# Kernel optimization log

Measured on AMD Instinct MI355X. Metric: run time of the kernel, lower is better.

Reference implementation:

```python
import jax, jax.numpy as jnp
import numpy as np

WS = 8  # window size
NH = 8  # num heads
LN_EPS = 1e-5


def _rel_pos_index(ws):
    coords = np.stack(np.meshgrid(np.arange(ws), np.arange(ws), indexing='ij'))  # [2,ws,ws]
    cf = coords.reshape(2, -1)                      # [2, ws*ws]
    rc = (cf[:, :, None] - cf[:, None, :]).transpose(1, 2, 0).astype(np.int64)  # [N,N,2]
    rc[..., 0] += ws - 1
    rc[..., 1] += ws - 1
    rc[..., 0] *= 2 * ws - 1
    return jnp.asarray(rc.sum(-1), dtype=jnp.int32)  # [N,N]


def setup_inputs() -> dict:
    key = jax.random.key(0)
    B, C, H, W = 8, 256, 128, 128
    hid = 4 * C
    ks = jax.random.split(key, 16)
    rn = lambda k, shape, s=0.02: (jax.random.normal(k, shape, jnp.float32) * s)
    return {
        'x': jax.random.normal(ks[0], (B, H * W, C), jnp.float32),
        'feature': jax.random.normal(ks[1], (B, C, H, W), jnp.float32),
        'Wq': rn(ks[2], (C, C)), 'bq': jnp.zeros((C,), jnp.float32),
        'Wk': rn(ks[3], (C, C)), 'bk': jnp.zeros((C,), jnp.float32),
        'Wv': rn(ks[4], (C, C)), 'bv': jnp.zeros((C,), jnp.float32),
        'Wo': rn(ks[5], (C, C)), 'bo': jnp.zeros((C,), jnp.float32),
        'rpb_table': rn(ks[6], ((2 * WS - 1) ** 2, NH)),
        'g1': jnp.ones((C,), jnp.float32), 'beta1': jnp.zeros((C,), jnp.float32),
        'g2': jnp.ones((C,), jnp.float32), 'beta2': jnp.zeros((C,), jnp.float32),
        'Wm1': rn(ks[7], (C, hid)), 'bm1': jnp.zeros((hid,), jnp.float32),
        'Wm2': rn(ks[8], (hid, C)), 'bm2': jnp.zeros((C,), jnp.float32),
        'Wu1': rn(ks[9], (C, C)), 'bu1': jnp.zeros((C,), jnp.float32),
        'Wu2': rn(ks[10], (C, C)), 'bu2': jnp.zeros((C,), jnp.float32),
        'rel_idx': _rel_pos_index(WS),
    }


def _gelu(t):
    return jax.nn.gelu(t, approximate=False)  # torch nn.GELU default (erf)


def _ln(t, g, b):
    mu = jnp.mean(t, axis=-1, keepdims=True)
    var = jnp.var(t, axis=-1, keepdims=True)
    return (t - mu) * jax.lax.rsqrt(var + LN_EPS) * g + b


def reference(x, feature, Wq, bq, Wk, bk, Wv, bv, Wo, bo, rpb_table,
              g1, beta1, g2, beta2, Wm1, bm1, Wm2, bm2, Wu1, bu1, Wu2, bu2,
              rel_idx):
    B, C, H, W = feature.shape
    ws, nh = WS, NH
    hd = C // nh
    scale = hd ** -0.5

    # unary potential: Linear -> GELU -> Linear on x [B, HW, C]
    unary = _gelu(x @ Wu1 + bu1) @ Wu2 + bu2

    # window partition of feature
    f = feature.reshape(B, C, H * W).transpose(0, 2, 1)  # [B, HW, C]
    pad_h = (-H) % ws
    pad_w = (-W) % ws
    fimg = f.reshape(B, H, W, C)
    if pad_h or pad_w:
        fimg = jnp.pad(fimg, ((0, 0), (0, pad_h), (0, pad_w), (0, 0)))
    Hp, Wp_ = H + pad_h, W + pad_w
    win = fimg.reshape(B, Hp // ws, ws, Wp_ // ws, ws, C)
    win = win.transpose(0, 1, 3, 2, 4, 5).reshape(-1, ws * ws, C)  # [nW, N, C]

    xn = _ln(win, g1, beta1)
    N = ws * ws
    q = (xn @ Wq + bq).reshape(-1, N, nh, hd).transpose(0, 2, 1, 3)  # [nW, h, N, d]
    k = (xn @ Wk + bk).reshape(-1, N, nh, hd).transpose(0, 2, 1, 3)
    v = (xn @ Wv + bv).reshape(-1, N, nh, hd).transpose(0, 2, 1, 3)

    attn = jnp.einsum('whnd,whmd->whnm', q, k) * scale
    bias = rpb_table[rel_idx.reshape(-1)].reshape(N, N, nh).transpose(2, 0, 1)  # [h,N,N]
    attn = jax.nn.softmax(attn + bias[None], axis=-1)
    o = jnp.einsum('whnm,whmd->whnd', attn, v)
    o = o.transpose(0, 2, 1, 3).reshape(-1, N, C) @ Wo + bo  # [nW, N, C]

    # window reverse
    rev = o.reshape(B, Hp // ws, Wp_ // ws, ws, ws, C)
    rev = rev.transpose(0, 1, 3, 2, 4, 5).reshape(B, Hp, Wp_, C)
    if pad_h or pad_w:
        rev = rev[:, :H, :W, :]
    rev = rev.reshape(B, H * W, C)

    x2 = unary + rev
    out = x2 + (_gelu(_ln(x2, g2, beta2) @ Wm1 + bm1) @ Wm2 + bm2)
    return out
```

## Files before the change

kernel.cpp:

```cpp
#include <hip/hip_runtime.h>
#include <cmath>


typedef unsigned short u16;
typedef unsigned int u32;
typedef __bf16 bf16x8 __attribute__((ext_vector_type(8)));
typedef float f32x4 __attribute__((ext_vector_type(4)));

#define EPI_NONE 0
#define EPI_GELU 1
#define EPI_WINREV 2
#define EPI_ADD 3

#define MTOK 131072
#define CC 256
#define HWC 16384

__device__ __forceinline__ float b2f(u16 u) {
    union { u32 i; float f; } x; x.i = ((u32)u) << 16; return x.f;
}
__device__ __forceinline__ u16 f2b(float f) {
    union { float f; u32 i; } x; x.f = f;
    u32 r = x.i + 0x7fffu + ((x.i >> 16) & 1u);
    return (u16)(r >> 16);
}
__device__ __forceinline__ u32 cvtpk(float lo, float hi) {
    u32 r;
    asm("v_cvt_pk_bf16_f32 %0, %1, %2" : "=v"(r) : "v"(lo), "v"(hi));
    return r;
}
__device__ __forceinline__ float gelu_f(float v) {
    return 0.5f * v * (1.0f + erff(v * 0.7071067811865475f));
}
__device__ __forceinline__ u32 ln_word(u32 w, float rs, float nmurs) {
    union { u32 i; float f; } lo, hi;
    lo.i = w << 16; hi.i = w & 0xffff0000u;
    return cvtpk(fmaf(lo.f, rs, nmurs), fmaf(hi.f, rs, nmurs));
}

__global__ __launch_bounds__(256) void transpose_f32_bf16(
    const float* __restrict__ src, const float* __restrict__ scale,
    u16* __restrict__ dst, int K, int N)
{
    __shared__ float t[32][33];
    const int k0 = blockIdx.x * 32, n0 = blockIdx.y * 32;
    const int tx = threadIdx.x & 31, ty = threadIdx.x >> 5;
    for (int i = ty; i < 32; i += 8) {
        float sc = scale ? scale[k0 + i] : 1.0f;
        t[i][tx] = src[(long)(k0 + i) * N + n0 + tx] * sc;
    }
    __syncthreads();
    for (int i = ty; i < 32; i += 8)
        dst[(long)(n0 + i) * K + k0 + tx] = f2b(t[tx][i]);
}

__global__ __launch_bounds__(256) void bias_fold(
    const float* __restrict__ W, const float* __restrict__ b,
    const float* __restrict__ beta, float* __restrict__ out, int K, int N)
{
    int n = blockIdx.x * 256 + threadIdx.x;
    if (n >= N) return;
    float s = b[n];
    for (int k = 0; k < K; k++) s += beta[k] * W[(long)k * N + n];
    out[n] = s;
}

__global__ __launch_bounds__(256) void rpb_gather(
    const float* __restrict__ rpb, const int* __restrict__ rel, float* __restrict__ outb)
{
    int e = blockIdx.x * 256 + threadIdx.x;
    int h = e >> 12, idx = e & 4095;
    int mi = idx >> 10, ni = (idx >> 8) & 3, lane = (idx >> 2) & 63, r = idx & 3;
    int row = mi * 16 + (lane >> 4) * 4 + r;
    int tok = 4 * (lane & 15) + ni;
    outb[e] = 1.4426950408889634f * rpb[rel[row * 64 + tok] * 8 + h];
}

__global__ __launch_bounds__(256) void ln_stats(
    const float* __restrict__ feat, float* __restrict__ muP, float* __restrict__ rsP)
{
    __shared__ float red1[4][256];
    __shared__ float red2[4][256];
    const int blk = blockIdx.x;
    const int b = blk >> 6, h2 = blk & 63;
    const int t = threadIdx.x;
    const int c_off = t >> 6, lane = t & 63;
    const int rl = lane >> 5, w4 = (lane & 31) * 4;
    const int tok0 = rl * 128 + w4;
    const float* fp = feat + (long)b * 256 * HWC + (long)(h2 * 2 + rl) * 128 + w4;
    float s1[4] = {0.f, 0.f, 0.f, 0.f};
    float s2[4] = {0.f, 0.f, 0.f, 0.f};
#pragma unroll 4
    for (int it = 0; it < 64; it++) {
        int c = it * 4 + c_off;
        float4 f = *(const float4*)(fp + (long)c * HWC);
        s1[0] += f.x; s2[0] += f.x * f.x;
        s1[1] += f.y; s2[1] += f.y * f.y;
        s1[2] += f.z; s2[2] += f.z * f.z;
        s1[3] += f.w; s2[3] += f.w * f.w;
    }
    *(float4*)&red1[c_off][tok0] = *(float4*)s1;
    *(float4*)&red2[c_off][tok0] = *(float4*)s2;
    __syncthreads();
    float a = red1[0][t] + red1[1][t] + red1[2][t] + red1[3][t];
    float q = red2[0][t] + red2[1][t] + red2[2][t] + red2[3][t];
    float mu = a * (1.f / 256.f);
    float var = q * (1.f / 256.f) - mu * mu;
    long tg = (long)b * HWC + h2 * 256 + t;
    muP[tg] = mu;
    rsP[tg] = rsqrtf(var + 1e-5f);
}

__global__ __launch_bounds__(256) void ln_transpose(
    const float* __restrict__ feat, const float* __restrict__ muP,
    const float* __restrict__ rsP, u16* __restrict__ xn)
{
    __shared__ u16 ct[64 * 258];
    const int blk = blockIdx.x;
    const int b = blk >> 6, h2 = blk & 63;
    const int t = threadIdx.x;
    const int c_off = t >> 6, lane = t & 63;
    const int rl = lane >> 5, w4 = (lane & 31) * 4;
    const int tok0 = rl * 128 + w4;
    const long tokg0 = (long)b * HWC + h2 * 256;
    const float4 mu4 = *(const float4*)(muP + tokg0 + tok0);
    const float4 rs4 = *(const float4*)(rsP + tokg0 + tok0);
    const float* fp = feat + (long)b * 256 * HWC + (long)(h2 * 2 + rl) * 128 + w4;
    const int koff = t & 3;

    for (int ch = 0; ch < 4; ch++) {
#pragma unroll
        for (int it = 0; it < 16; it++) {
            int c = ch * 64 + it * 4 + c_off;
            float4 f = *(const float4*)(fp + (long)c * HWC);
            uint2 pk;
            pk.x = cvtpk((f.x - mu4.x) * rs4.x, (f.y - mu4.y) * rs4.y);
            pk.y = cvtpk((f.z - mu4.z) * rs4.z, (f.w - mu4.w) * rs4.w);
            *(uint2*)&ct[(it * 4 + c_off) * 258 + tok0] = pk;
        }
        __syncthreads();
#pragma unroll
        for (int p = 0; p < 4; p++) {
            int token = p * 64 + (t >> 2);
            int hh = h2 * 2 + (token >> 7), wc = token & 127;
            long orow = ((long)b * 256 + (hh >> 3) * 16 + (wc >> 3)) * 64
                      + (hh & 7) * 8 + (wc & 7);
            union { uint4 q[2]; u16 u[16]; } pkk;
#pragma unroll
            for (int cc = 0; cc < 16; cc++)
                pkk.u[cc] = ct[(koff * 16 + cc) * 258 + token];
            u16* op = xn + orow * 256 + ch * 64 + koff * 16;
            *(uint4*)(op) = pkk.q[0];
            *(uint4*)(op + 8) = pkk.q[1];
        }
        __syncthreads();
    }
}

__global__ __launch_bounds__(256) void ln2_stats(
    const u16* __restrict__ x, float* __restrict__ mu, float* __restrict__ rs)
{
    const int wave = threadIdx.x >> 6, lane = threadIdx.x & 63;
    const long row = (long)blockIdx.x * 4 + wave;
    union { uint2 v; u16 u[4]; } pk;
    pk.v = *(const uint2*)(x + row * 256 + lane * 4);
    float v0 = b2f(pk.u[0]), v1 = b2f(pk.u[1]), v2 = b2f(pk.u[2]), v3 = b2f(pk.u[3]);
    float s1 = v0 + v1 + v2 + v3;
    float s2 = v0 * v0 + v1 * v1 + v2 * v2 + v3 * v3;
    for (int off = 1; off < 64; off <<= 1) {
        s1 += __shfl_xor(s1, off);
        s2 += __shfl_xor(s2, off);
    }
    if (lane == 0) {
        float m = s1 * (1.f / 256.f);
        float var = s2 * (1.f / 256.f) - m * m;
        mu[row] = m;
        rs[row] = rsqrtf(var + 1e-5f);
    }
}

template <int EPI, bool OUTF32, int ASRC, bool SPLIT3>
__global__ __launch_bounds__(256) void gemm_core(
    const void* __restrict__ Av, const u16* __restrict__ BT,
    const float* __restrict__ bias, void* __restrict__ out0,
    void* __restrict__ out1, void* __restrict__ out2,
    const u16* __restrict__ res, const float* __restrict__ muA,
    const float* __restrict__ rsA, int M, int N, int K)
{
    __shared__ u16 As[128 * 32];
    __shared__ u16 Bs[128 * 32];
    const int tid = threadIdx.x;
    const int n0 = blockIdx.x * 128;
    const int m0 = blockIdx.y * 128;
    const int wave = tid >> 6, lane = tid & 63;
    const int wm = wave >> 1, wn = wave & 1;
    const int quad = lane >> 4, l16 = lane & 15;

    f32x4 acc[4][4];
#pragma unroll
    for (int i = 0; i < 4; i++)
#pragma unroll
        for (int j = 0; j < 4; j++) acc[i][j] = (f32x4){0.f, 0.f, 0.f, 0.f};

    const int srow = wave * 32 + (lane >> 2);
    const int gch = ((lane & 3) ^ ((lane >> 3) & 3)) * 8;
    const u16* gB = BT + (long)(n0 + srow) * K + gch;
    u16* lB = &Bs[srow * 32 + (lane & 3) * 8];

    const u16* gA0 = nullptr; u16* lA = nullptr;
    const float* gAf = nullptr; const u16* gAh = nullptr;
    u16 *sA0 = nullptr, *sA1 = nullptr;
    float rsv = 0.f, nmu = 0.f;
    const int ar = tid >> 1;
    const int aseg = (tid & 1) * 2;
    const int ao = (tid >> 2) & 3;
    if constexpr (ASRC == 0) {
        gA0 = (const u16*)Av + (long)(m0 + srow) * K + gch;
        lA = &As[srow * 32 + (lane & 3) * 8];
    } else {
        sA0 = &As[ar * 32 + (aseg ^ ao) * 8];
        sA1 = &As[ar * 32 + ((aseg + 1) ^ ao) * 8];
        if constexpr (ASRC == 1) {
            gAf = (const float*)Av + (long)(m0 + ar) * K + aseg * 8;
        } else {
            gAh = (const u16*)Av + (long)(m0 + ar) * K + aseg * 8;
            rsv = rsA[m0 + ar];
            nmu = -muA[m0 + ar] * rsv;
        }
    }

    const int rdsw = ((l16 >> 1) & 3);

    for (int k0 = 0; k0 < K; k0 += 32) {
        float4 a0, a1, a2, a3;
        uint4 u0, u1v;
        if constexpr (ASRC == 1) {
            a0 = *(const float4*)(gAf + k0);
            a1 = *(const float4*)(gAf + k0 + 4);
            a2 = *(const float4*)(gAf + k0 + 8);
            a3 = *(const float4*)(gAf + k0 + 12);
        } else if constexpr (ASRC == 2) {
            u0 = *(const uint4*)(gAh + k0);
            u1v = *(const uint4*)(gAh + k0 + 8);
        }
        __syncthreads();
        if constexpr (ASRC == 0) {
            __builtin_amdgcn_global_load_lds(
                (const __attribute__((address_space(1))) void*)(gA0 + k0),
                (__attribute__((address_space(3))) void*)lA, 16, 0, 0);
            __builtin_amdgcn_global_load_lds(
                (const __attribute__((address_space(1))) void*)(gA0 + k0 + 16 * K),
                (__attribute__((address_space(3))) void*)(lA + 16 * 32), 16, 0, 0);
        } else if constexpr (ASRC == 1) {
            uint4 w0 = {cvtpk(a0.x, a0.y), cvtpk(a0.z, a0.w),
                        cvtpk(a1.x, a1.y), cvtpk(a1.z, a1.w)};
            uint4 w1 = {cvtpk(a2.x, a2.y), cvtpk(a2.z, a2.w),
                        cvtpk(a3.x, a3.y), cvtpk(a3.z, a3.w)};
            *(uint4*)sA0 = w0;
            *(uint4*)sA1 = w1;
        } else {
            uint4 w0 = {ln_word(u0.x, rsv, nmu), ln_word(u0.y, rsv, nmu),
                        ln_word(u0.z, rsv, nmu), ln_word(u0.w, rsv, nmu)};
            uint4 w1 = {ln_word(u1v.x, rsv, nmu), ln_word(u1v.y, rsv, nmu),
                        ln_word(u1v.z, rsv, nmu), ln_word(u1v.w, rsv, nmu)};
            *(uint4*)sA0 = w0;
            *(uint4*)sA1 = w1;
        }
        __builtin_amdgcn_global_load_lds(
            (const __attribute__((address_space(1))) void*)(gB + k0),
            (__attribute__((address_space(3))) void*)lB, 16, 0, 0);
        __builtin_amdgcn_global_load_lds(
            (const __attribute__((address_space(1))) void*)(gB + k0 + 16 * K),
            (__attribute__((address_space(3))) void*)(lB + 16 * 32), 16, 0, 0);
        __syncthreads();
        bf16x8 af[4], bfr[4];
#pragma unroll
        for (int mi = 0; mi < 4; mi++)
            af[mi] = *(const bf16x8*)&As[(wm * 64 + mi * 16 + l16) * 32 + ((quad ^ rdsw) * 8)];
#pragma unroll
        for (int ni = 0; ni < 4; ni++)
            bfr[ni] = *(const bf16x8*)&Bs[(wn * 64 + ni * 16 + l16) * 32 + ((quad ^ rdsw) * 8)];
#pragma unroll
        for (int mi = 0; mi < 4; mi++)
#pragma unroll
            for (int ni = 0; ni < 4; ni++)
                acc[mi][ni] = __builtin_amdgcn_mfma_f32_16x16x32_bf16(
                    bfr[ni], af[mi], acc[mi][ni], 0, 0, 0);
    }

#pragma unroll
    for (int mi = 0; mi < 4; mi++) {
        const int row = m0 + wm * 64 + mi * 16 + l16;
        long orow;
        if constexpr (EPI == EPI_WINREV) {
            int wI = row >> 6, n = row & 63;
            int bI = wI >> 8, rem = wI & 255;
            int wh = rem >> 4, wwI = rem & 15;
            orow = (long)bI * HWC + (long)((wh * 8 + (n >> 3)) * 128 + wwI * 8 + (n & 7));
        } else {
            orow = row;
        }
#pragma unroll
        for (int ni = 0; ni < 4; ni++) {
            const int cb = n0 + wn * 64 + ni * 16 + quad * 4;
            float4 bb = *(const float4*)(bias + cb);
            float v0 = acc[mi][ni][0] + bb.x;
            float v1 = acc[mi][ni][1] + bb.y;
            float v2 = acc[mi][ni][2] + bb.z;
            float v3 = acc[mi][ni][3] + bb.w;
            if constexpr (EPI == EPI_GELU) {
                v0 = gelu_f(v0); v1 = gelu_f(v1);
                v2 = gelu_f(v2); v3 = gelu_f(v3);
            }
            if constexpr (EPI == EPI_WINREV || EPI == EPI_ADD) {
                uint2 rr = *(const uint2*)(res + orow * (long)N + cb);
                v0 += b2f((u16)(rr.x & 0xffff));
                v1 += b2f((u16)(rr.x >> 16));
                v2 += b2f((u16)(rr.y & 0xffff));
                v3 += b2f((u16)(rr.y >> 16));
            }
            if constexpr (SPLIT3) {
                u16* ob = (u16*)(n0 < 256 ? out0 : n0 < 512 ? out1 : out2);
                uint2 o;
                o.x = cvtpk(v0, v1);
                o.y = cvtpk(v2, v3);
                *(uint2*)(ob + orow * 256L + (cb & 255)) = o;
            } else if constexpr (OUTF32) {
                float4 o = {v0, v1, v2, v3};
                *(float4*)((float*)out0 + orow * (long)N + cb) = o;
            } else {
                uint2 o;
                o.x = cvtpk(v0, v1);
                o.y = cvtpk(v2, v3);
                *(uint2*)((u16*)out0 + orow * (long)N + cb) = o;
            }
        }
    }
}

__global__ __launch_bounds__(256, 3) void attn_kernel(
    const u16* __restrict__ qb, const u16* __restrict__ kb,
    const u16* __restrict__ vb, const float* __restrict__ biasp,
    u16* __restrict__ ob)
{
    __shared__ u16 lds[4 * 6400];
    const int wave = threadIdx.x >> 6, lane = threadIdx.x & 63;
    const int quad = lane >> 4, l16 = lane & 15;
    const int w = blockIdx.x >> 1;
    const int h = ((blockIdx.x & 1) << 2) + wave;
    u16* Pl = lds + wave * 6400;
    u16* VT = Pl + 4096;
    const long base = (long)w * 64 * 256 + h * 32;

    bf16x8 aq[4], bk4[4];
#pragma unroll
    for (int mi = 0; mi < 4; mi++)
        aq[mi] = *(const bf16x8*)(qb + base + (long)(mi * 16 + l16) * 256 + quad * 8);
#pragma unroll
    for (int ni = 0; ni < 4; ni++)
        bk4[ni] = *(const bf16x8*)(kb + base + (long)(4 * l16 + ni) * 256 + quad * 8);

    {
        const int t = lane;
        const int s = ((t >> 4) & 1) * 32 + ((t >> 2) & 3) * 8 + (t >> 5) * 4 + (t & 3);
        const u16* vp = vb + base + (long)t * 256;
        union { uint4 v; u16 u[8]; } p0, p1, p2, p3;
        p0.v = *(const uint4*)(vp);
        p1.v = *(const uint4*)(vp + 8);
        p2.v = *(const uint4*)(vp + 16);
        p3.v = *(const uint4*)(vp + 24);
#pragma unroll
        for (int j = 0; j < 8; j++) {
            VT[j * 72 + s]        = p0.u[j];
            VT[(8 + j) * 72 + s]  = p1.u[j];
            VT[(16 + j) * 72 + s] = p2.u[j];
            VT[(24 + j) * 72 + s] = p3.u[j];
        }
    }

    f32x4 s[4][4];
#pragma unroll
    for (int i = 0; i < 4; i++)
#pragma unroll
        for (int j = 0; j < 4; j++) s[i][j] = (f32x4){0.f, 0.f, 0.f, 0.f};
    __builtin_amdgcn_s_setprio(1);
#pragma unroll
    for (int mi = 0; mi < 4; mi++)
#pragma unroll
        for (int ni = 0; ni < 4; ni++)
            s[mi][ni] = __builtin_amdgcn_mfma_f32_16x16x32_bf16(aq[mi], bk4[ni], s[mi][ni], 0, 0, 0);
    __builtin_amdgcn_s_setprio(0);

    const float* bp = biasp + h * 4096;
    const float SC2 = 0.17677669529663687f * 1.4426950408889634f;
    const int pq = l16 & 3, pks = (l16 >> 2) & 1, ph = l16 >> 3;
#pragma unroll
    for (int mi = 0; mi < 4; mi++) {
        f32x4 bb[4];
#pragma unroll
        for (int ni = 0; ni < 4; ni++)
            bb[ni] = *(const f32x4*)(bp + ((mi * 4 + ni) << 8) + lane * 4);
#pragma unroll
        for (int r = 0; r < 4; r++) {
            float p[4];
#pragma unroll
            for (int ni = 0; ni < 4; ni++)
                p[ni] = __builtin_amdgcn_exp2f(s[mi][ni][r] * SC2 + bb[ni][r]);
            float sum = (p[0] + p[1]) + (p[2] + p[3]);
            for (int off = 1; off < 16; off <<= 1) sum += __shfl_xor(sum, off);
            float inv = __builtin_amdgcn_rcpf(sum);
            int mrow = mi * 16 + quad * 4 + r;
            uint2 w2;
            w2.x = cvtpk(p[0] * inv, p[1] * inv);
            w2.y = cvtpk(p[2] * inv, p[3] * inv);
            *(uint2*)&Pl[pks * 2048 + mrow * 32 + pq * 8 + ph * 4] = w2;
        }
    }

    f32x4 o4[2][4];
#pragma unroll
    for (int i = 0; i < 2; i++)
#pragma unroll
        for (int j = 0; j < 4; j++) o4[i][j] = (f32x4){0.f, 0.f, 0.f, 0.f};
#pragma unroll
    for (int ks = 0; ks < 2; ks++) {
        bf16x8 at[2], pb[4];
#pragma unroll
        for (int mi = 0; mi < 2; mi++)
            at[mi] = *(const bf16x8*)&VT[(mi * 16 + l16) * 72 + ks * 32 + quad * 8];
#pragma unroll
        for (int nt = 0; nt < 4; nt++)
            pb[nt] = *(const bf16x8*)&Pl[ks * 2048 + (nt * 16 + l16) * 32 + quad * 8];
        __builtin_amdgcn_s_setprio(1);
#pragma unroll
        for (int mi = 0; mi < 2; mi++)
#pragma unroll
            for (int nt = 0; nt < 4; nt++)
                o4[mi][nt] = __builtin_amdgcn_mfma_f32_16x16x32_bf16(at[mi], pb[nt], o4[mi][nt], 0, 0, 0);
        __builtin_amdgcn_s_setprio(0);
    }

#pragma unroll
    for (int nt = 0; nt < 4; nt++)
#pragma unroll
        for (int mi = 0; mi < 2; mi++) {
            uint2 w2;
            w2.x = cvtpk(o4[mi][nt][0], o4[mi][nt][1]);
            w2.y = cvtpk(o4[mi][nt][2], o4[mi][nt][3]);
            *(uint2*)(ob + base + (long)(nt * 16 + l16) * 256 + mi * 16 + quad * 4) = w2;
        }
}

extern "C" void kernel_launch(void* const* d_in, const int* in_sizes, int n_in,
                              void* d_out, int out_size, void* d_ws, size_t ws_size,
                              hipStream_t stream)
{
    (void)in_sizes; (void)n_in; (void)out_size; (void)ws_size;
    const float* x    = (const float*)d_in[0];
    const float* feat = (const float*)d_in[1];
    const float* Wq = (const float*)d_in[2];   const float* bq = (const float*)d_in[3];
    const float* Wk = (const float*)d_in[4];   const float* bk = (const float*)d_in[5];
    const float* Wv = (const float*)d_in[6];   const float* bv = (const float*)d_in[7];
    const float* Wo = (const float*)d_in[8];   const float* bo = (const float*)d_in[9];
    const float* rpb = (const float*)d_in[10];
    const float* g1 = (const float*)d_in[11];  const float* be1 = (const float*)d_in[12];
    const float* g2 = (const float*)d_in[13];  const float* be2 = (const float*)d_in[14];
    const float* Wm1 = (const float*)d_in[15]; const float* bm1 = (const float*)d_in[16];
    const float* Wm2 = (const float*)d_in[17]; const float* bm2 = (const float*)d_in[18];
    const float* Wu1 = (const float*)d_in[19]; const float* bu1 = (const float*)d_in[20];
    const float* Wu2 = (const float*)d_in[21]; const float* bu2 = (const float*)d_in[22];
    const int* rel = (const int*)d_in[23];
    float* outp = (float*)d_out;

    char* ws = (char*)d_ws;
    u16* WqT  = (u16*)(ws);
    u16* WkT  = WqT + 65536;
    u16* WvT  = WkT + 65536;
    u16* WoT  = WvT + 65536;
    u16* Wu1T = WoT + 65536;
    u16* Wu2T = Wu1T + 65536;
    u16* Wm1T = Wu2T + 65536;
    u16* Wm2T = Wm1T + 262144;
    float* biasf = (float*)(ws + 1835008);
    float* bqkv  = (float*)(ws + 1966080);
    float* bm1f  = (float*)(ws + 1970176);
    const long MB = 1024L * 1024;
    u16* S0 = (u16*)(ws + 2 * MB);
    u16* S1 = (u16*)(ws + 66 * MB);
    u16* S2 = (u16*)(ws + 130 * MB);
    u16* xn  = (u16*)d_out;
    float* muP = (float*)((char*)d_out + 96 * MB);
    float* rsP = (float*)((char*)d_out + 97 * MB);
    u16* qb  = S0;
    u16* kb  = S1;
    u16* vb  = S2;
    u16* O   = S0;
    u16* u1h = S2;
    u16* un  = S1;
    u16* x2  = S2;
    float* mu2 = (float*)S0;
    float* rs2 = mu2 + MTOK;
    u16* hch = S1;

    const dim3 blk(256);

    transpose_f32_bf16<<<dim3(8, 8), blk, 0, stream>>>(Wq, g1, WqT, 256, 256);
    transpose_f32_bf16<<<dim3(8, 8), blk, 0, stream>>>(Wk, g1, WkT, 256, 256);
    transpose_f32_bf16<<<dim3(8, 8), blk, 0, stream>>>(Wv, g1, WvT, 256, 256);
    transpose_f32_bf16<<<dim3(8, 8), blk, 0, stream>>>(Wo, nullptr, WoT, 256, 256);
    transpose_f32_bf16<<<dim3(8, 8), blk, 0, stream>>>(Wu1, nullptr, Wu1T, 256, 256);
    transpose_f32_bf16<<<dim3(8, 8), blk, 0, stream>>>(Wu2, nullptr, Wu2T, 256, 256);
    transpose_f32_bf16<<<dim3(8, 32), blk, 0, stream>>>(Wm1, g2, Wm1T, 256, 1024);
    transpose_f32_bf16<<<dim3(32, 8), blk, 0, stream>>>(Wm2, nullptr, Wm2T, 1024, 256);
    bias_fold<<<dim3(1), blk, 0, stream>>>(Wq, bq, be1, bqkv, 256, 256);
    bias_fold<<<dim3(1), blk, 0, stream>>>(Wk, bk, be1, bqkv + 256, 256, 256);
    bias_fold<<<dim3(1), blk, 0, stream>>>(Wv, bv, be1, bqkv + 512, 256, 256);
    bias_fold<<<dim3(4), blk, 0, stream>>>(Wm1, bm1, be2, bm1f, 256, 1024);
    rpb_gather<<<dim3(128), blk, 0, stream>>>(rpb, rel, biasf);

    ln_stats<<<dim3(512), blk, 0, stream>>>(feat, muP, rsP);
    ln_transpose<<<dim3(512), blk, 0, stream>>>(feat, muP, rsP, xn);

    gemm_core<EPI_NONE, false, 0, true><<<dim3(6, 1024), blk, 0, stream>>>(
        xn, WqT, bqkv, qb, kb, vb, nullptr, nullptr, nullptr, MTOK, 768, 256);

    attn_kernel<<<dim3(4096), blk, 0, stream>>>(qb, kb, vb, biasf, O);

    gemm_core<EPI_GELU, false, 1, false><<<dim3(2, 1024), blk, 0, stream>>>(
        x, Wu1T, bu1, u1h, nullptr, nullptr, nullptr, nullptr, nullptr, MTOK, 256, 256);
    gemm_core<EPI_NONE, false, 0, false><<<dim3(2, 1024), blk, 0, stream>>>(
        u1h, Wu2T, bu2, un, nullptr, nullptr, nullptr, nullptr, nullptr, MTOK, 256, 256);

    gemm_core<EPI_WINREV, false, 0, false><<<dim3(2, 1024), blk, 0, stream>>>(
        O, WoT, bo, x2, nullptr, nullptr, un, nullptr, nullptr, MTOK, 256, 256);

    ln2_stats<<<dim3(32768), blk, 0, stream>>>(x2, mu2, rs2);
    for (int ch = 0; ch < 4; ch++) {
        const u16* x2c = x2 + (long)ch * 32768 * 256;
        float* outc = outp + (long)ch * 32768 * 256;
        gemm_core<EPI_GELU, false, 2, false><<<dim3(8, 256), blk, 0, stream>>>(
            x2c, Wm1T, bm1f, hch, nullptr, nullptr, nullptr,
            mu2 + (long)ch * 32768, rs2 + (long)ch * 32768, 32768, 1024, 256);
        gemm_core<EPI_ADD, true, 0, false><<<dim3(2, 256), blk, 0, stream>>>(
            hch, Wm2T, bm2, outc, nullptr, nullptr, x2c, nullptr, nullptr, 32768, 256, 1024);
    }
}
```

Baseline: 1.353 ms.

## Double-buffer GEMM LDS tiles and remap workgroups across XCDs

```diff
diff --git a/kernel.cpp b/kernel.cpp
--- a/kernel.cpp
+++ b/kernel.cpp
@@ -185,13 +185,15 @@
     const float* __restrict__ bias, void* __restrict__ out0,
     void* __restrict__ out1, void* __restrict__ out2,
     const u16* __restrict__ res, const float* __restrict__ muA,
-    const float* __restrict__ rsA, int M, int N, int K)
-{
-    __shared__ u16 As[128 * 32];
-    __shared__ u16 Bs[128 * 32];
+    const float* __restrict__ rsA, int M, int N, int K, int nx)
+{
+    __shared__ u16 As[2][128 * 32];
+    __shared__ u16 Bs[2][128 * 32];
     const int tid = threadIdx.x;
-    const int n0 = blockIdx.x * 128;
-    const int m0 = blockIdx.y * 128;
+    const int nwg = gridDim.x;
+    const int lg = ((int)blockIdx.x & 7) * (nwg >> 3) + ((int)blockIdx.x >> 3);
+    const int n0 = (lg % nx) * 128;
+    const int m0 = (lg / nx) * 128;
     const int wave = tid >> 6, lane = tid & 63;
     const int wm = wave >> 1, wn = wave & 1;
     const int quad = lane >> 4, l16 = lane & 15;
@@ -205,21 +207,20 @@
     const int srow = wave * 32 + (lane >> 2);
     const int gch = ((lane & 3) ^ ((lane >> 3) & 3)) * 8;
     const u16* gB = BT + (long)(n0 + srow) * K + gch;
-    u16* lB = &Bs[srow * 32 + (lane & 3) * 8];
-
-    const u16* gA0 = nullptr; u16* lA = nullptr;
+    const int lBoff = srow * 32 + (lane & 3) * 8;
+
+    const u16* gA0 = nullptr;
     const float* gAf = nullptr; const u16* gAh = nullptr;
-    u16 *sA0 = nullptr, *sA1 = nullptr;
+    int sA0off = 0, sA1off = 0;
     float rsv = 0.f, nmu = 0.f;
     const int ar = tid >> 1;
     const int aseg = (tid & 1) * 2;
     const int ao = (tid >> 2) & 3;
     if constexpr (ASRC == 0) {
         gA0 = (const u16*)Av + (long)(m0 + srow) * K + gch;
-        lA = &As[srow * 32 + (lane & 3) * 8];
     } else {
-        sA0 = &As[ar * 32 + (aseg ^ ao) * 8];
-        sA1 = &As[ar * 32 + ((aseg + 1) ^ ao) * 8];
+        sA0off = ar * 32 + (aseg ^ ao) * 8;
+        sA1off = ar * 32 + ((aseg + 1) ^ ao) * 8;
         if constexpr (ASRC == 1) {
             gAf = (const float*)Av + (long)(m0 + ar) * K + aseg * 8;
         } else {
@@ -231,61 +232,105 @@
 
     const int rdsw = ((l16 >> 1) & 3);
 
+    if constexpr (ASRC == 0) {
+        __builtin_amdgcn_global_load_lds(
+            (const __attribute__((address_space(1))) void*)(gA0),
+            (__attribute__((address_space(3))) void*)&As[0][lBoff], 16, 0, 0);
+        __builtin_amdgcn_global_load_lds(
+            (const __attribute__((address_space(1))) void*)(gA0 + 16 * K),
+            (__attribute__((address_space(3))) void*)&As[0][lBoff + 16 * 32], 16, 0, 0);
+    } else if constexpr (ASRC == 1) {
+        float4 a0 = *(const float4*)(gAf);
+        float4 a1 = *(const float4*)(gAf + 4);
+        float4 a2 = *(const float4*)(gAf + 8);
+        float4 a3 = *(const float4*)(gAf + 12);
+        uint4 w0 = {cvtpk(a0.x, a0.y), cvtpk(a0.z, a0.w),
+                    cvtpk(a1.x, a1.y), cvtpk(a1.z, a1.w)};
+        uint4 w1 = {cvtpk(a2.x, a2.y), cvtpk(a2.z, a2.w),
+                    cvtpk(a3.x, a3.y), cvtpk(a3.z, a3.w)};
+        *(uint4*)&As[0][sA0off] = w0;
+        *(uint4*)&As[0][sA1off] = w1;
+    } else {
+        uint4 u0 = *(const uint4*)(gAh);
+        uint4 u1v = *(const uint4*)(gAh + 8);
+        uint4 w0 = {ln_word(u0.x, rsv, nmu), ln_word(u0.y, rsv, nmu),
+                    ln_word(u0.z, rsv, nmu), ln_word(u0.w, rsv, nmu)};
+        uint4 w1 = {ln_word(u1v.x, rsv, nmu), ln_word(u1v.y, rsv, nmu),
+                    ln_word(u1v.z, rsv, nmu), ln_word(u1v.w, rsv, nmu)};
+        *(uint4*)&As[0][sA0off] = w0;
+        *(uint4*)&As[0][sA1off] = w1;
+    }
+    __builtin_amdgcn_global_load_lds(
+        (const __attribute__((address_space(1))) void*)(gB),
+        (__attribute__((address_space(3))) void*)&Bs[0][lBoff], 16, 0, 0);
+    __builtin_amdgcn_global_load_lds(
+        (const __attribute__((address_space(1))) void*)(gB + 16 * K),
+        (__attribute__((address_space(3))) void*)&Bs[0][lBoff + 16 * 32], 16, 0, 0);
+    __syncthreads();
+
+    int cur = 0;
+#pragma unroll 2
     for (int k0 = 0; k0 < K; k0 += 32) {
+        const int kn = k0 + 32;
+        const bool hn = kn < K;
         float4 a0, a1, a2, a3;
         uint4 u0, u1v;
-        if constexpr (ASRC == 1) {
-            a0 = *(const float4*)(gAf + k0);
-            a1 = *(const float4*)(gAf + k0 + 4);
-            a2 = *(const float4*)(gAf + k0 + 8);
-            a3 = *(const float4*)(gAf + k0 + 12);
-        } else if constexpr (ASRC == 2) {
-            u0 = *(const uint4*)(gAh + k0);
-            u1v = *(const uint4*)(gAh + k0 + 8);
-        }
-        __syncthreads();
-        if constexpr (ASRC == 0) {
+        if (hn) {
+            if constexpr (ASRC == 0) {
+                __builtin_amdgcn_global_load_lds(
+                    (const __attribute__((address_space(1))) void*)(gA0 + kn),
+                    (__attribute__((address_space(3))) void*)&As[cur ^ 1][lBoff], 16, 0, 0);
+                __builtin_amdgcn_global_load_lds(
+                    (const __attribute__((address_space(1))) void*)(gA0 + kn + 16 * K),
+                    (__attribute__((address_space(3))) void*)&As[cur ^ 1][lBoff + 16 * 32], 16, 0, 0);
+            } else if constexpr (ASRC == 1) {
+                a0 = *(const float4*)(gAf + kn);
+                a1 = *(const float4*)(gAf + kn + 4);
+                a2 = *(const float4*)(gAf + kn + 8);
+                a3 = *(const float4*)(gAf + kn + 12);
+            } else if constexpr (ASRC == 2) {
+                u0 = *(const uint4*)(gAh + kn);
+                u1v = *(const uint4*)(gAh + kn + 8);
+            }
             __builtin_amdgcn_global_load_lds(
-                (const __attribute__((address_space(1))) void*)(gA0 + k0),
-                (__attribute__((address_space(3))) void*)lA, 16, 0, 0);
+                (const __attribute__((address_space(1))) void*)(gB + kn),
+                (__attribute__((address_space(3))) void*)&Bs[cur ^ 1][lBoff], 16, 0, 0);
             __builtin_amdgcn_global_load_lds(
-                (const __attribute__((address_space(1))) void*)(gA0 + k0 + 16 * K),
-                (__attribute__((address_space(3))) void*)(lA + 16 * 32), 16, 0, 0);
-        } else if constexpr (ASRC == 1) {
-            uint4 w0 = {cvtpk(a0.x, a0.y), cvtpk(a0.z, a0.w),
-                        cvtpk(a1.x, a1.y), cvtpk(a1.z, a1.w)};
-            uint4 w1 = {cvtpk(a2.x, a2.y), cvtpk(a2.z, a2.w),
-                        cvtpk(a3.x, a3.y), cvtpk(a3.z, a3.w)};
-            *(uint4*)sA0 = w0;
-            *(uint4*)sA1 = w1;
-        } else {
-            uint4 w0 = {ln_word(u0.x, rsv, nmu), ln_word(u0.y, rsv, nmu),
-                        ln_word(u0.z, rsv, nmu), ln_word(u0.w, rsv, nmu)};
-            uint4 w1 = {ln_word(u1v.x, rsv, nmu), ln_word(u1v.y, rsv, nmu),
-                        ln_word(u1v.z, rsv, nmu), ln_word(u1v.w, rsv, nmu)};
-            *(uint4*)sA0 = w0;
-            *(uint4*)sA1 = w1;
-        }
-        __builtin_amdgcn_global_load_lds(
-            (const __attribute__((address_space(1))) void*)(gB + k0),
-            (__attribute__((address_space(3))) void*)lB, 16, 0, 0);
-        __builtin_amdgcn_global_load_lds(
-            (const __attribute__((address_space(1))) void*)(gB + k0 + 16 * K),
-            (__attribute__((address_space(3))) void*)(lB + 16 * 32), 16, 0, 0);
-        __syncthreads();
+                (const __attribute__((address_space(1))) void*)(gB + kn + 16 * K),
+                (__attribute__((address_space(3))) void*)&Bs[cur ^ 1][lBoff + 16 * 32], 16, 0, 0);
+        }
         bf16x8 af[4], bfr[4];
 #pragma unroll
         for (int mi = 0; mi < 4; mi++)
-            af[mi] = *(const bf16x8*)&As[(wm * 64 + mi * 16 + l16) * 32 + ((quad ^ rdsw) * 8)];
+            af[mi] = *(const bf16x8*)&As[cur][(wm * 64 + mi * 16 + l16) * 32 + ((quad ^ rdsw) * 8)];
 #pragma unroll
         for (int ni = 0; ni < 4; ni++)
-            bfr[ni] = *(const bf16x8*)&Bs[(wn * 64 + ni * 16 + l16) * 32 + ((quad ^ rdsw) * 8)];
+            bfr[ni] = *(const bf16x8*)&Bs[cur][(wn * 64 + ni * 16 + l16) * 32 + ((quad ^ rdsw) * 8)];
 #pragma unroll
         for (int mi = 0; mi < 4; mi++)
 #pragma unroll
             for (int ni = 0; ni < 4; ni++)
                 acc[mi][ni] = __builtin_amdgcn_mfma_f32_16x16x32_bf16(
                     bfr[ni], af[mi], acc[mi][ni], 0, 0, 0);
+        if (hn) {
+            if constexpr (ASRC == 1) {
+                uint4 w0 = {cvtpk(a0.x, a0.y), cvtpk(a0.z, a0.w),
+                            cvtpk(a1.x, a1.y), cvtpk(a1.z, a1.w)};
+                uint4 w1 = {cvtpk(a2.x, a2.y), cvtpk(a2.z, a2.w),
+                            cvtpk(a3.x, a3.y), cvtpk(a3.z, a3.w)};
+                *(uint4*)&As[cur ^ 1][sA0off] = w0;
+                *(uint4*)&As[cur ^ 1][sA1off] = w1;
+            } else if constexpr (ASRC == 2) {
+                uint4 w0 = {ln_word(u0.x, rsv, nmu), ln_word(u0.y, rsv, nmu),
+                            ln_word(u0.z, rsv, nmu), ln_word(u0.w, rsv, nmu)};
+                uint4 w1 = {ln_word(u1v.x, rsv, nmu), ln_word(u1v.y, rsv, nmu),
+                            ln_word(u1v.z, rsv, nmu), ln_word(u1v.w, rsv, nmu)};
+                *(uint4*)&As[cur ^ 1][sA0off] = w0;
+                *(uint4*)&As[cur ^ 1][sA1off] = w1;
+            }
+        }
+        __syncthreads();
+        cur ^= 1;
     }
 
 #pragma unroll
@@ -521,27 +566,27 @@
     ln_stats<<<dim3(512), blk, 0, stream>>>(feat, muP, rsP);
     ln_transpose<<<dim3(512), blk, 0, stream>>>(feat, muP, rsP, xn);
 
-    gemm_core<EPI_NONE, false, 0, true><<<dim3(6, 1024), blk, 0, stream>>>(
-        xn, WqT, bqkv, qb, kb, vb, nullptr, nullptr, nullptr, MTOK, 768, 256);
+    gemm_core<EPI_NONE, false, 0, true><<<dim3(6144), blk, 0, stream>>>(
+        xn, WqT, bqkv, qb, kb, vb, nullptr, nullptr, nullptr, MTOK, 768, 256, 6);
 
     attn_kernel<<<dim3(4096), blk, 0, stream>>>(qb, kb, vb, biasf, O);
 
-    gemm_core<EPI_GELU, false, 1, false><<<dim3(2, 1024), blk, 0, stream>>>(
-        x, Wu1T, bu1, u1h, nullptr, nullptr, nullptr, nullptr, nullptr, MTOK, 256, 256);
-    gemm_core<EPI_NONE, false, 0, false><<<dim3(2, 1024), blk, 0, stream>>>(
-        u1h, Wu2T, bu2, un, nullptr, nullptr, nullptr, nullptr, nullptr, MTOK, 256, 256);
-
-    gemm_core<EPI_WINREV, false, 0, false><<<dim3(2, 1024), blk, 0, stream>>>(
-        O, WoT, bo, x2, nullptr, nullptr, un, nullptr, nullptr, MTOK, 256, 256);
+    gemm_core<EPI_GELU, false, 1, false><<<dim3(2048), blk, 0, stream>>>(
+        x, Wu1T, bu1, u1h, nullptr, nullptr, nullptr, nullptr, nullptr, MTOK, 256, 256, 2);
+    gemm_core<EPI_NONE, false, 0, false><<<dim3(2048), blk, 0, stream>>>(
+        u1h, Wu2T, bu2, un, nullptr, nullptr, nullptr, nullptr, nullptr, MTOK, 256, 256, 2);
+
+    gemm_core<EPI_WINREV, false, 0, false><<<dim3(2048), blk, 0, stream>>>(
+        O, WoT, bo, x2, nullptr, nullptr, un, nullptr, nullptr, MTOK, 256, 256, 2);
 
     ln2_stats<<<dim3(32768), blk, 0, stream>>>(x2, mu2, rs2);
     for (int ch = 0; ch < 4; ch++) {
         const u16* x2c = x2 + (long)ch * 32768 * 256;
         float* outc = outp + (long)ch * 32768 * 256;
-        gemm_core<EPI_GELU, false, 2, false><<<dim3(8, 256), blk, 0, stream>>>(
+        gemm_core<EPI_GELU, false, 2, false><<<dim3(2048), blk, 0, stream>>>(
             x2c, Wm1T, bm1f, hch, nullptr, nullptr, nullptr,
-            mu2 + (long)ch * 32768, rs2 + (long)ch * 32768, 32768, 1024, 256);
-        gemm_core<EPI_ADD, true, 0, false><<<dim3(2, 256), blk, 0, stream>>>(
-            hch, Wm2T, bm2, outc, nullptr, nullptr, x2c, nullptr, nullptr, 32768, 256, 1024);
-    }
-}
+            mu2 + (long)ch * 32768, rs2 + (long)ch * 32768, 32768, 1024, 256, 8);
+        gemm_core<EPI_ADD, true, 0, false><<<dim3(512), blk, 0, stream>>>(
+            hch, Wm2T, bm2, outc, nullptr, nullptr, x2c, nullptr, nullptr, 32768, 256, 1024, 2);
+    }
+}
```

Result: faster. 1.304 ms (-3.6%).
